# Performance work log

Hardware: AMD Instinct MI355X
Metric: run time of the kernel (lower is better)

## Reference

```python
import jax, jax.numpy as jnp
import numpy as np

N = 100_000      # nodes
E = 600_000      # edges (before self-loops)
F_IN = 128       # in_channels
H0, H1 = 64, 128 # hidden_channels
D = 512          # FLAGS.D
G = 512          # number of graphs in batch
OUT = 1          # FLAGS.out_dim


def _lin(key, fan_in, fan_out):
    k1, k2 = jax.random.split(key)
    s = 1.0 / np.sqrt(fan_in)
    return (jax.random.uniform(k1, (fan_in, fan_out), jnp.float32, -s, s),
            jax.random.uniform(k2, (fan_out,), jnp.float32, -s, s))


def setup_inputs() -> dict:
    key = jax.random.key(0)
    ks = jax.random.split(key, 12)
    x = jax.random.normal(ks[0], (N, F_IN), jnp.float32)
    src = jax.random.randint(ks[1], (E,), 0, N, jnp.int32)
    dst = jax.random.randint(ks[2], (E,), 0, N, jnp.int32)
    batch = jnp.sort(jax.random.randint(ks[3], (N,), 0, G, jnp.int32))
    Wc0, bc0 = _lin(ks[4], F_IN, H0)   # GCNConv 1
    Wc1, bc1 = _lin(ks[5], H0, H1)     # GCNConv 2
    Wf, bf = _lin(ks[6], H1, D)        # first_MLP: Linear(128, D)
    Wh0, bh0 = _lin(ks[7], D, D // 2)  # MLP head hidden layers
    Wh1, bh1 = _lin(ks[8], D // 2, D // 4)
    Wh2, bh2 = _lin(ks[9], D // 4, D // 8)
    Wo, bo = _lin(ks[10], D // 8, OUT) # MLP head output
    return dict(x=x, src=src, dst=dst, batch=batch,
                Wc0=Wc0, bc0=bc0, Wc1=Wc1, bc1=bc1, Wf=Wf, bf=bf,
                Wh0=Wh0, bh0=bh0, Wh1=Wh1, bh1=bh1, Wh2=Wh2, bh2=bh2,
                Wo=Wo, bo=bo)


def gcn_conv(x, src, dst, W, b):
    """PyG GCNConv: add self-loops, sym-normalized neighbor sum, then bias."""
    n = x.shape[0]
    loop = jnp.arange(n, dtype=src.dtype)
    s = jnp.concatenate([src, loop])
    d = jnp.concatenate([dst, loop])
    deg = jax.ops.segment_sum(jnp.ones(s.shape[0], x.dtype), d, num_segments=n)
    dinv = jnp.where(deg > 0, jax.lax.rsqrt(deg), 0.0)
    h = x @ W                                  # [n, out]
    coeff = (dinv[s] * dinv[d])[:, None]       # [e+n, 1]
    out = jax.ops.segment_sum(h[s] * coeff, d, num_segments=n)
    return out + b


def reference(x, src, dst, batch, Wc0, bc0, Wc1, bc1, Wf, bf,
              Wh0, bh0, Wh1, bh1, Wh2, bh2, Wo, bo):
    # two GCNConv layers + ReLU (dropout p=0.0 is a no-op)
    h = jax.nn.relu(gcn_conv(x, src, dst, Wc0, bc0))
    h = jax.nn.relu(gcn_conv(h, src, dst, Wc1, bc1))
    # global mean pool over graphs
    cnt = jax.ops.segment_sum(jnp.ones(h.shape[0], h.dtype), batch, num_segments=G)
    g = jax.ops.segment_sum(h, batch, num_segments=G) / jnp.maximum(cnt, 1.0)[:, None]
    # first_MLP (plain Linear) then MLP head with ReLU hidden layers
    e = g @ Wf + bf
    e = jax.nn.relu(e @ Wh0 + bh0)
    e = jax.nn.relu(e @ Wh1 + bh1)
    e = jax.nn.relu(e @ Wh2 + bh2)
    out = e @ Wo + bo
    return out
```

## Files before the change

### kernel.cpp

```cpp
#include <hip/hip_runtime.h>
#include <hip/hip_bf16.h>

#define NN   100000
#define NE   600000
#define FIN  128
#define H0   64
#define H1   128
#define NG   512
#define BM   64

__global__ void hist_kernel(const int* __restrict__ idx, int* __restrict__ cnt, int n)
{
    int i = blockIdx.x * blockDim.x + threadIdx.x;
    int stride = gridDim.x * blockDim.x;
    for (; i < n; i += stride) atomicAdd(&cnt[idx[i]], 1);
}

__global__ void batch_count_kernel(const int* __restrict__ batch,
                                   int* __restrict__ cnt, int n)
{
    const int g = blockIdx.x * blockDim.x + threadIdx.x;
    if (g >= NG) return;
    int lo = 0, hi = n;
    while (lo < hi) { const int m = (lo + hi) >> 1; if (batch[m] < g) lo = m + 1; else hi = m; }
    const int start = lo;
    lo = 0; hi = n;
    while (lo < hi) { const int m = (lo + hi) >> 1; if (batch[m] < g + 1) lo = m + 1; else hi = m; }
    cnt[g] = lo - start;
}

__global__ void dinv_kernel(const int* __restrict__ deg, float* __restrict__ dinv, int n)
{
    int i = blockIdx.x * blockDim.x + threadIdx.x;
    if (i < n) dinv[i] = 1.0f / sqrtf((float)(deg[i] + 1));
}

__global__ __launch_bounds__(256) void scan1_kernel(
    const int* __restrict__ deg, int* __restrict__ rp, int* __restrict__ bsum, int n)
{
    __shared__ int tmp[256];
    const int t = threadIdx.x;
    const int i = blockIdx.x * 256 + t;
    int v = (i < n) ? deg[i] : 0;
    tmp[t] = v;
    __syncthreads();
    #pragma unroll
    for (int off = 1; off < 256; off <<= 1) {
        int a = (t >= off) ? tmp[t - off] : 0;
        __syncthreads();
        tmp[t] += a;
        __syncthreads();
    }
    if (i < n) rp[i] = tmp[t] - v;
    if (t == 255) bsum[blockIdx.x] = tmp[255];
}

__global__ __launch_bounds__(512) void scan2_kernel(
    const int* __restrict__ bsum, int* __restrict__ boff, int nb)
{
    __shared__ int tmp[512];
    const int t = threadIdx.x;
    int v = (t < nb) ? bsum[t] : 0;
    tmp[t] = v;
    __syncthreads();
    #pragma unroll
    for (int off = 1; off < 512; off <<= 1) {
        int a = (t >= off) ? tmp[t - off] : 0;
        __syncthreads();
        tmp[t] += a;
        __syncthreads();
    }
    if (t < nb) boff[t] = tmp[t] - v;
}

__global__ __launch_bounds__(256) void scan3_kernel(
    int* __restrict__ rp, int* __restrict__ wcur, const int* __restrict__ boff, int n)
{
    const int i = blockIdx.x * 256 + threadIdx.x;
    if (i < n) {
        const int v = rp[i] + boff[blockIdx.x];
        rp[i] = v;
        wcur[i] = v;
    }
}

__global__ void fill_kernel(const int* __restrict__ src, const int* __restrict__ dst,
                            int* __restrict__ wcur, int* __restrict__ csr, int ne)
{
    int i = blockIdx.x * blockDim.x + threadIdx.x;
    const int stride = gridDim.x * blockDim.x;
    for (; i < ne; i += stride) {
        const int d = dst[i];
        const int p = atomicAdd(&wcur[d], 1);
        csr[p] = src[i];
    }
}

__global__ __launch_bounds__(512) void gemm1_kernel(
    const float* __restrict__ x, const float* __restrict__ W,
    const float* __restrict__ dinv, float* __restrict__ h0s, int n)
{
    __shared__ float Wl[FIN * H0];
    __shared__ float xs[BM * FIN];
    const int t = threadIdx.x;
    for (int i = t; i < FIN * H0 / 4; i += 512)
        ((float4*)Wl)[i] = ((const float4*)W)[i];

    const int lane = t & 63;
    const int w    = t >> 6;
    const int ntiles = (n + BM - 1) / BM;

    for (int tile = blockIdx.x; tile < ntiles; tile += gridDim.x) {
        const int row0  = tile * BM;
        const int nrows = min(BM, n - row0);
        __syncthreads();
        {
            const float4* xg = (const float4*)(x + (size_t)row0 * FIN);
            const int nf4 = nrows * FIN / 4;
            #pragma unroll
            for (int i = 0; i < 4; ++i) {
                const int idx = t + i * 512;
                if (idx < nf4) ((float4*)xs)[idx] = xg[idx];
            }
        }
        __syncthreads();

        float acc[8] = {0.f,0.f,0.f,0.f,0.f,0.f,0.f,0.f};
        const float* xw = xs + (w * 8) * FIN;
        #pragma unroll 2
        for (int k = 0; k < FIN; k += 4) {
            const float w0 = Wl[(k + 0) * H0 + lane];
            const float w1 = Wl[(k + 1) * H0 + lane];
            const float w2 = Wl[(k + 2) * H0 + lane];
            const float w3 = Wl[(k + 3) * H0 + lane];
            #pragma unroll
            for (int r = 0; r < 8; ++r) {
                const float4 xv = *(const float4*)(xw + r * FIN + k);
                acc[r] += xv.x * w0; acc[r] += xv.y * w1;
                acc[r] += xv.z * w2; acc[r] += xv.w * w3;
            }
        }
        const int rbase = row0 + w * 8;
        #pragma unroll
        for (int r = 0; r < 8; ++r) {
            const int row = rbase + r;
            if (row < n) h0s[(size_t)row * H0 + lane] = acc[r] * dinv[row];
        }
    }
}

template <int MODE>
__global__ __launch_bounds__(256) void gather_kernel(
    const float* __restrict__ hin, const int* __restrict__ rowptr,
    const int* __restrict__ deg, const int* __restrict__ csr,
    const float* __restrict__ dinv, const float* __restrict__ bias,
    float* __restrict__ hout, int n)
{
    const int lane = threadIdx.x & 63;
    int wid = (blockIdx.x * blockDim.x + threadIdx.x) >> 6;
    const int nw = (gridDim.x * blockDim.x) >> 6;
    for (int d = wid; d < n; d += nw) {
        const int r0  = rowptr[d];
        const int cnt = deg[d];
        float acc = hin[(size_t)d * H0 + lane];
        int k = 0;
        for (; k + 1 < cnt; k += 2) {
            const int s0 = csr[r0 + k];
            const int s1 = csr[r0 + k + 1];
            acc += hin[(size_t)s0 * H0 + lane];
            acc += hin[(size_t)s1 * H0 + lane];
        }
        if (k < cnt) acc += hin[(size_t)csr[r0 + k] * H0 + lane];
        const float dv = dinv[d];
        if (MODE == 0)
            hout[(size_t)d * H0 + lane] = fmaxf(acc * dv + bias[lane], 0.f) * dv;
        else
            hout[(size_t)d * H0 + lane] = acc * dv;
    }
}

__global__ __launch_bounds__(512) void gemm2_pool_kernel(
    const float* __restrict__ a , const float* __restrict__ W ,
    const float* __restrict__ bc1, const int* __restrict__ batch,
    float* __restrict__ gsum, int n)
{
    __shared__ float Wl[H0 * H1];
    __shared__ float xs[BM * H0];
    __shared__ float red[4][H1];
    __shared__ int   bs[BM];
    const int t = threadIdx.x;
    for (int i = t; i < H0 * H1 / 4; i += 512)
        ((float4*)Wl)[i] = ((const float4*)W)[i];

    const int lane = t & 63;
    const int w    = t >> 6;
    const int ch   = w & 1;
    const int rg   = w >> 1;
    const int col  = ch * 64 + lane;
    const float bj = bc1[col];
    const int ntiles = (n + BM - 1) / BM;

    for (int tile = blockIdx.x; tile < ntiles; tile += gridDim.x) {
        const int row0  = tile * BM;
        const int nrows = min(BM, n - row0);
        __syncthreads();
        {
            const float4* ag = (const float4*)(a + (size_t)row0 * H0);
            const int nf4 = nrows * H0 / 4;
            #pragma unroll
            for (int i = 0; i < 2; ++i) {
                const int idx = t + i * 512;
                if (idx < nf4) ((float4*)xs)[idx] = ag[idx];
            }
            if (t < nrows) bs[t] = batch[row0 + t];
        }
        __syncthreads();

        float acc[16];
        #pragma unroll
        for (int r = 0; r < 16; ++r) acc[r] = 0.f;
        const float* xw = xs + (rg * 16) * H0;
        #pragma unroll 2
        for (int k = 0; k < H0; k += 4) {
            const float w0 = Wl[(k + 0) * H1 + col];
            const float w1 = Wl[(k + 1) * H1 + col];
            const float w2 = Wl[(k + 2) * H1 + col];
            const float w3 = Wl[(k + 3) * H1 + col];
            #pragma unroll
            for (int r = 0; r < 16; ++r) {
                const float4 xv = *(const float4*)(xw + r * H0 + k);
                acc[r] += xv.x * w0; acc[r] += xv.y * w1;
                acc[r] += xv.z * w2; acc[r] += xv.w * w3;
            }
        }

        const bool uni = (nrows == BM) && (bs[0] == bs[BM - 1]);
        if (uni) {
            float s = 0.f;
            #pragma unroll
            for (int r = 0; r < 16; ++r) s += fmaxf(acc[r] + bj, 0.f);
            red[rg][col] = s;
            __syncthreads();
            if (rg == 0)
                atomicAdd(&gsum[(size_t)bs[0] * H1 + col],
                          red[0][col] + red[1][col] + red[2][col] + red[3][col]);
        } else {
            int gcur = -1; float run = 0.f;
            #pragma unroll
            for (int r = 0; r < 16; ++r) {
                const int row = rg * 16 + r;
                if (row < nrows) {
                    const int g = bs[row];
                    const float v = fmaxf(acc[r] + bj, 0.f);
                    if (g != gcur) {
                        if (gcur >= 0) atomicAdd(&gsum[(size_t)gcur * H1 + col], run);
                        gcur = g; run = v;
                    } else run += v;
                }
            }
            if (gcur >= 0) atomicAdd(&gsum[(size_t)gcur * H1 + col], run);
        }
    }
}

__global__ __launch_bounds__(256) void mlp_kernel(
    const float* __restrict__ gsum, const int* __restrict__ cnt,
    const float* __restrict__ Wf,  const float* __restrict__ bf,
    const float* __restrict__ Wh0, const float* __restrict__ bh0,
    const float* __restrict__ Wh1, const float* __restrict__ bh1,
    const float* __restrict__ Wh2, const float* __restrict__ bh2,
    const float* __restrict__ Wo,  const float* __restrict__ bo,
    float* __restrict__ out)
{
    __shared__ float gm[128];
    __shared__ float e0[512];
    __shared__ float e1[256];
    __shared__ float e2[128];
    __shared__ float e3[64];
    const int gi = blockIdx.x;
    const int t  = threadIdx.x;

    if (t < 128) {
        const int c = cnt[gi];
        gm[t] = gsum[gi * 128 + t] * (1.0f / (float)max(c, 1));
    }
    __syncthreads();

    for (int jj = t; jj < 512; jj += 256) {
        float acc = bf[jj];
        for (int k = 0; k < 128; ++k) acc += gm[k] * Wf[k * 512 + jj];
        e0[jj] = acc;
    }
    __syncthreads();

    {
        float acc = bh0[t];
        for (int k = 0; k < 512; ++k) acc += e0[k] * Wh0[k * 256 + t];
        if (t < 256) e1[t] = fmaxf(acc, 0.f);
    }
    __syncthreads();

    if (t < 128) {
        float acc = bh1[t];
        for (int k = 0; k < 256; ++k) acc += e1[k] * Wh1[k * 128 + t];
        e2[t] = fmaxf(acc, 0.f);
    }
    __syncthreads();

    if (t < 64) {
        float acc = bh2[t];
        for (int k = 0; k < 128; ++k) acc += e2[k] * Wh2[k * 64 + t];
        e3[t] = fmaxf(acc, 0.f);
    }
    __syncthreads();

    if (t < 64) {
        float p = e3[t] * Wo[t];
        #pragma unroll
        for (int off = 32; off > 0; off >>= 1) p += __shfl_down(p, off);
        if (t == 0) out[gi] = p + bo[0];
    }
}

extern "C" void kernel_launch(void* const* d_in, const int* in_sizes, int n_in,
                              void* d_out, int out_size, void* d_ws, size_t ws_size,
                              hipStream_t stream)
{
    const float* x    = (const float*)d_in[0];
    const int*   src  = (const int*)  d_in[1];
    const int*   dst  = (const int*)  d_in[2];
    const int*   batch= (const int*)  d_in[3];
    const float* Wc0  = (const float*)d_in[4];
    const float* bc0  = (const float*)d_in[5];
    const float* Wc1  = (const float*)d_in[6];
    const float* bc1  = (const float*)d_in[7];
    const float* Wf   = (const float*)d_in[8];
    const float* bf   = (const float*)d_in[9];
    const float* Wh0  = (const float*)d_in[10];
    const float* bh0  = (const float*)d_in[11];
    const float* Wh1  = (const float*)d_in[12];
    const float* bh1  = (const float*)d_in[13];
    const float* Wh2  = (const float*)d_in[14];
    const float* bh2  = (const float*)d_in[15];
    const float* Wo   = (const float*)d_in[16];
    const float* bo   = (const float*)d_in[17];
    float* out = (float*)d_out;

    const int n = NN, ne = NE;
    const int nblk = (n + 255) / 256;

    char* ws = (char*)d_ws;
    size_t off = 0;
    auto alloc = [&](size_t bytes) {
        void* p = ws + off;
        off = (off + bytes + 255) & ~(size_t)255;
        return p;
    };
    int*   deg    = (int*)  alloc((size_t)n * 4);
    float* dinv   = (float*)alloc((size_t)n * 4);
    int*   rowptr = (int*)  alloc((size_t)n * 4);
    int*   wcur   = (int*)  alloc((size_t)n * 4);
    int*   bsum   = (int*)  alloc(512 * 4);
    int*   boff   = (int*)  alloc(512 * 4);
    int*   csr    = (int*)  alloc((size_t)ne * 4);
    float* h0s    = (float*)alloc((size_t)n * H0 * 4);
    float* h1s    = (float*)alloc((size_t)n * H0 * 4);
    float* agg1   = (float*)alloc((size_t)n * H0 * 4);
    float* gsum   = (float*)alloc((size_t)NG * H1 * 4);
    int*   cnt    = (int*)  alloc((size_t)NG * 4);

    hipMemsetAsync(deg,  0, (size_t)n * 4, stream);
    hipMemsetAsync(gsum, 0, (size_t)NG * H1 * 4, stream);

    hist_kernel<<<1024, 256, 0, stream>>>(dst, deg, ne);
    batch_count_kernel<<<2, 256, 0, stream>>>(batch, cnt, n);
    dinv_kernel<<<nblk, 256, 0, stream>>>(deg, dinv, n);

    scan1_kernel<<<nblk, 256, 0, stream>>>(deg, rowptr, bsum, n);
    scan2_kernel<<<1, 512, 0, stream>>>(bsum, boff, nblk);
    scan3_kernel<<<nblk, 256, 0, stream>>>(rowptr, wcur, boff, n);
    fill_kernel<<<1024, 256, 0, stream>>>(src, dst, wcur, csr, ne);

    gemm1_kernel<<<512, 512, 0, stream>>>(x, Wc0, dinv, h0s, n);
    gather_kernel<0><<<4096, 256, 0, stream>>>(h0s, rowptr, deg, csr, dinv, bc0, h1s, n);

    gather_kernel<1><<<4096, 256, 0, stream>>>(h1s, rowptr, deg, csr, dinv, bc0, agg1, n);
    gemm2_pool_kernel<<<768, 512, 0, stream>>>(agg1, Wc1, bc1, batch, gsum, n);

    mlp_kernel<<<NG, 256, 0, stream>>>(gsum, cnt, Wf, bf, Wh0, bh0,
                                       Wh1, bh1, Wh2, bh2, Wo, bo, out);
}
```

Baseline: 428.9 us.

## Use 4x4/4x8 register tiles in both GEMM kernels with 256-thread blocks

```diff
diff --git a/kernel.cpp b/kernel.cpp
--- a/kernel.cpp
+++ b/kernel.cpp
@@ -96,18 +96,21 @@
     }
 }
 
-__global__ __launch_bounds__(512) void gemm1_kernel(
+__global__ __launch_bounds__(256) void gemm1_kernel(
     const float* __restrict__ x, const float* __restrict__ W,
     const float* __restrict__ dinv, float* __restrict__ h0s, int n)
 {
     __shared__ float Wl[FIN * H0];
     __shared__ float xs[BM * FIN];
     const int t = threadIdx.x;
-    for (int i = t; i < FIN * H0 / 4; i += 512)
+    for (int i = t; i < FIN * H0 / 4; i += 256)
         ((float4*)Wl)[i] = ((const float4*)W)[i];
 
     const int lane = t & 63;
     const int w    = t >> 6;
+    const int rsub = lane >> 4;
+    const int j0   = (lane & 15) * 4;
+    const int wrow = w * 16 + rsub * 4;
     const int ntiles = (n + BM - 1) / BM;
 
     for (int tile = blockIdx.x; tile < ntiles; tile += gridDim.x) {
@@ -117,34 +120,42 @@
         {
             const float4* xg = (const float4*)(x + (size_t)row0 * FIN);
             const int nf4 = nrows * FIN / 4;
+            for (int idx = t; idx < nf4; idx += 256)
+                ((float4*)xs)[idx] = xg[idx];
+        }
+        __syncthreads();
+
+        float acc[4][4] = {};
+        const float* xr = xs + wrow * FIN;
+        #pragma unroll 4
+        for (int k = 0; k < FIN; k += 4) {
+            const float4 w0 = *(const float4*)&Wl[(k + 0) * H0 + j0];
+            const float4 w1 = *(const float4*)&Wl[(k + 1) * H0 + j0];
+            const float4 w2 = *(const float4*)&Wl[(k + 2) * H0 + j0];
+            const float4 w3 = *(const float4*)&Wl[(k + 3) * H0 + j0];
             #pragma unroll
-            for (int i = 0; i < 4; ++i) {
-                const int idx = t + i * 512;
-                if (idx < nf4) ((float4*)xs)[idx] = xg[idx];
-            }
-        }
-        __syncthreads();
-
-        float acc[8] = {0.f,0.f,0.f,0.f,0.f,0.f,0.f,0.f};
-        const float* xw = xs + (w * 8) * FIN;
-        #pragma unroll 2
-        for (int k = 0; k < FIN; k += 4) {
-            const float w0 = Wl[(k + 0) * H0 + lane];
-            const float w1 = Wl[(k + 1) * H0 + lane];
-            const float w2 = Wl[(k + 2) * H0 + lane];
-            const float w3 = Wl[(k + 3) * H0 + lane];
-            #pragma unroll
-            for (int r = 0; r < 8; ++r) {
-                const float4 xv = *(const float4*)(xw + r * FIN + k);
-                acc[r] += xv.x * w0; acc[r] += xv.y * w1;
-                acc[r] += xv.z * w2; acc[r] += xv.w * w3;
-            }
-        }
-        const int rbase = row0 + w * 8;
+            for (int r = 0; r < 4; ++r) {
+                const float4 xv = *(const float4*)&xr[r * FIN + k];
+                acc[r][0] += xv.x * w0.x; acc[r][0] += xv.y * w1.x;
+                acc[r][0] += xv.z * w2.x; acc[r][0] += xv.w * w3.x;
+                acc[r][1] += xv.x * w0.y; acc[r][1] += xv.y * w1.y;
+                acc[r][1] += xv.z * w2.y; acc[r][1] += xv.w * w3.y;
+                acc[r][2] += xv.x * w0.z; acc[r][2] += xv.y * w1.z;
+                acc[r][2] += xv.z * w2.z; acc[r][2] += xv.w * w3.z;
+                acc[r][3] += xv.x * w0.w; acc[r][3] += xv.y * w1.w;
+                acc[r][3] += xv.z * w2.w; acc[r][3] += xv.w * w3.w;
+            }
+        }
         #pragma unroll
-        for (int r = 0; r < 8; ++r) {
-            const int row = rbase + r;
-            if (row < n) h0s[(size_t)row * H0 + lane] = acc[r] * dinv[row];
+        for (int r = 0; r < 4; ++r) {
+            const int row = row0 + wrow + r;
+            if (row < n) {
+                const float dv = dinv[row];
+                float4 o;
+                o.x = acc[r][0] * dv; o.y = acc[r][1] * dv;
+                o.z = acc[r][2] * dv; o.w = acc[r][3] * dv;
+                *(float4*)&h0s[(size_t)row * H0 + j0] = o;
+            }
         }
     }
 }
@@ -179,25 +190,26 @@
     }
 }
 
-__global__ __launch_bounds__(512) void gemm2_pool_kernel(
+__global__ __launch_bounds__(256) void gemm2_pool_kernel(
     const float* __restrict__ a , const float* __restrict__ W ,
     const float* __restrict__ bc1, const int* __restrict__ batch,
     float* __restrict__ gsum, int n)
 {
     __shared__ float Wl[H0 * H1];
-    __shared__ float xs[BM * H0];
+    __shared__ float as[BM * H0];
     __shared__ float red[4][H1];
     __shared__ int   bs[BM];
     const int t = threadIdx.x;
-    for (int i = t; i < H0 * H1 / 4; i += 512)
+    for (int i = t; i < H0 * H1 / 4; i += 256)
         ((float4*)Wl)[i] = ((const float4*)W)[i];
 
     const int lane = t & 63;
     const int w    = t >> 6;
-    const int ch   = w & 1;
-    const int rg   = w >> 1;
-    const int col  = ch * 64 + lane;
-    const float bj = bc1[col];
+    const int rsub = lane >> 4;
+    const int j0   = (lane & 15) * 8;
+    const int wrow = w * 16 + rsub * 4;
+    const float4 bA = *(const float4*)&bc1[j0];
+    const float4 bB = *(const float4*)&bc1[j0 + 4];
     const int ntiles = (n + BM - 1) / BM;
 
     for (int tile = blockIdx.x; tile < ntiles; tile += gridDim.x) {
@@ -207,58 +219,90 @@
         {
             const float4* ag = (const float4*)(a + (size_t)row0 * H0);
             const int nf4 = nrows * H0 / 4;
+            for (int idx = t; idx < nf4; idx += 256)
+                ((float4*)as)[idx] = ag[idx];
+            if (t < nrows) bs[t] = batch[row0 + t];
+        }
+        __syncthreads();
+
+        float acc[4][8] = {};
+        const float* ar = as + wrow * H0;
+        #pragma unroll 4
+        for (int k = 0; k < H0; k += 4) {
+            float4 wa[4], wb[4];
             #pragma unroll
-            for (int i = 0; i < 2; ++i) {
-                const int idx = t + i * 512;
-                if (idx < nf4) ((float4*)xs)[idx] = ag[idx];
-            }
-            if (t < nrows) bs[t] = batch[row0 + t];
-        }
-        __syncthreads();
-
-        float acc[16];
-        #pragma unroll
-        for (int r = 0; r < 16; ++r) acc[r] = 0.f;
-        const float* xw = xs + (rg * 16) * H0;
-        #pragma unroll 2
-        for (int k = 0; k < H0; k += 4) {
-            const float w0 = Wl[(k + 0) * H1 + col];
-            const float w1 = Wl[(k + 1) * H1 + col];
-            const float w2 = Wl[(k + 2) * H1 + col];
-            const float w3 = Wl[(k + 3) * H1 + col];
+            for (int kk = 0; kk < 4; ++kk) {
+                wa[kk] = *(const float4*)&Wl[(k + kk) * H1 + j0];
+                wb[kk] = *(const float4*)&Wl[(k + kk) * H1 + j0 + 4];
+            }
             #pragma unroll
-            for (int r = 0; r < 16; ++r) {
-                const float4 xv = *(const float4*)(xw + r * H0 + k);
-                acc[r] += xv.x * w0; acc[r] += xv.y * w1;
-                acc[r] += xv.z * w2; acc[r] += xv.w * w3;
-            }
-        }
-
+            for (int r = 0; r < 4; ++r) {
+                const float4 xv = *(const float4*)&ar[r * H0 + k];
+                acc[r][0] += xv.x * wa[0].x; acc[r][0] += xv.y * wa[1].x;
+                acc[r][0] += xv.z * wa[2].x; acc[r][0] += xv.w * wa[3].x;
+                acc[r][1] += xv.x * wa[0].y; acc[r][1] += xv.y * wa[1].y;
+                acc[r][1] += xv.z * wa[2].y; acc[r][1] += xv.w * wa[3].y;
+                acc[r][2] += xv.x * wa[0].z; acc[r][2] += xv.y * wa[1].z;
+                acc[r][2] += xv.z * wa[2].z; acc[r][2] += xv.w * wa[3].z;
+                acc[r][3] += xv.x * wa[0].w; acc[r][3] += xv.y * wa[1].w;
+                acc[r][3] += xv.z * wa[2].w; acc[r][3] += xv.w * wa[3].w;
+                acc[r][4] += xv.x * wb[0].x; acc[r][4] += xv.y * wb[1].x;
+                acc[r][4] += xv.z * wb[2].x; acc[r][4] += xv.w * wb[3].x;
+                acc[r][5] += xv.x * wb[0].y; acc[r][5] += xv.y * wb[1].y;
+                acc[r][5] += xv.z * wb[2].y; acc[r][5] += xv.w * wb[3].y;
+                acc[r][6] += xv.x * wb[0].z; acc[r][6] += xv.y * wb[1].z;
+                acc[r][6] += xv.z * wb[2].z; acc[r][6] += xv.w * wb[3].z;
+                acc[r][7] += xv.x * wb[0].w; acc[r][7] += xv.y * wb[1].w;
+                acc[r][7] += xv.z * wb[2].w; acc[r][7] += xv.w * wb[3].w;
+            }
+        }
+
+        const float bv[8] = {bA.x, bA.y, bA.z, bA.w, bB.x, bB.y, bB.z, bB.w};
         const bool uni = (nrows == BM) && (bs[0] == bs[BM - 1]);
         if (uni) {
-            float s = 0.f;
+            float s[8];
             #pragma unroll
-            for (int r = 0; r < 16; ++r) s += fmaxf(acc[r] + bj, 0.f);
-            red[rg][col] = s;
+            for (int c = 0; c < 8; ++c) {
+                s[c] = fmaxf(acc[0][c] + bv[c], 0.f) + fmaxf(acc[1][c] + bv[c], 0.f)
+                     + fmaxf(acc[2][c] + bv[c], 0.f) + fmaxf(acc[3][c] + bv[c], 0.f);
+                s[c] += __shfl_xor(s[c], 16);
+                s[c] += __shfl_xor(s[c], 32);
+            }
+            if (rsub == 0) {
+                #pragma unroll
+                for (int c = 0; c < 8; ++c) red[w][j0 + c] = s[c];
+            }
             __syncthreads();
-            if (rg == 0)
-                atomicAdd(&gsum[(size_t)bs[0] * H1 + col],
-                          red[0][col] + red[1][col] + red[2][col] + red[3][col]);
+            if (t < H1)
+                atomicAdd(&gsum[(size_t)bs[0] * H1 + t],
+                          red[0][t] + red[1][t] + red[2][t] + red[3][t]);
         } else {
-            int gcur = -1; float run = 0.f;
+            int gcur = -1; float run[8];
             #pragma unroll
-            for (int r = 0; r < 16; ++r) {
-                const int row = rg * 16 + r;
+            for (int r = 0; r < 4; ++r) {
+                const int row = wrow + r;
                 if (row < nrows) {
                     const int g = bs[row];
-                    const float v = fmaxf(acc[r] + bj, 0.f);
                     if (g != gcur) {
-                        if (gcur >= 0) atomicAdd(&gsum[(size_t)gcur * H1 + col], run);
-                        gcur = g; run = v;
-                    } else run += v;
+                        if (gcur >= 0) {
+                            #pragma unroll
+                            for (int c = 0; c < 8; ++c)
+                                atomicAdd(&gsum[(size_t)gcur * H1 + j0 + c], run[c]);
+                        }
+                        gcur = g;
+                        #pragma unroll
+                        for (int c = 0; c < 8; ++c) run[c] = fmaxf(acc[r][c] + bv[c], 0.f);
+                    } else {
+                        #pragma unroll
+                        for (int c = 0; c < 8; ++c) run[c] += fmaxf(acc[r][c] + bv[c], 0.f);
+                    }
                 }
             }
-            if (gcur >= 0) atomicAdd(&gsum[(size_t)gcur * H1 + col], run);
+            if (gcur >= 0) {
+                #pragma unroll
+                for (int c = 0; c < 8; ++c)
+                    atomicAdd(&gsum[(size_t)gcur * H1 + j0 + c], run[c]);
+            }
         }
     }
 }
@@ -381,11 +425,11 @@
     scan3_kernel<<<nblk, 256, 0, stream>>>(rowptr, wcur, boff, n);
     fill_kernel<<<1024, 256, 0, stream>>>(src, dst, wcur, csr, ne);
 
-    gemm1_kernel<<<512, 512, 0, stream>>>(x, Wc0, dinv, h0s, n);
+    gemm1_kernel<<<1024, 256, 0, stream>>>(x, Wc0, dinv, h0s, n);
     gather_kernel<0><<<4096, 256, 0, stream>>>(h0s, rowptr, deg, csr, dinv, bc0, h1s, n);
 
     gather_kernel<1><<<4096, 256, 0, stream>>>(h1s, rowptr, deg, csr, dinv, bc0, agg1, n);
-    gemm2_pool_kernel<<<768, 512, 0, stream>>>(agg1, Wc1, bc1, batch, gsum, n);
+    gemm2_pool_kernel<<<1024, 256, 0, stream>>>(agg1, Wc1, bc1, batch, gsum, n);
 
     mlp_kernel<<<NG, 256, 0, stream>>>(gsum, cnt, Wf, bf, Wh0, bh0,
                                        Wh1, bh1, Wh2, bh2, Wo, bo, out);
```

Measured after the change: 415.9 us. 3.0% less time.
